# Kernel optimization log

Hardware: AMD Instinct MI355X
Metric: run time of the kernel (lower is better)

## Reference

```python
import jax, jax.numpy as jnp
import numpy as np

D, DK, DV, H, DFF = 1024, 64, 64, 16, 4096
B, LD, LE = 8, 1024, 1024
NEG = -1e9


def _ln(x, g, b, eps=1e-5):
    m = jnp.mean(x, axis=-1, keepdims=True)
    v = jnp.var(x, axis=-1, keepdims=True)
    return (x - m) / jnp.sqrt(v + eps) * g + b


def _mha(q_src, kv_src, wq, bq, wk, bk, wv, bv, mask):
    # wq/wk: [H, D, DK], wv: [H, D, DV]; per-head linear projections (with bias)
    Q = jnp.einsum('bld,hdk->bhlk', q_src, wq) + bq[:, None, :]
    K = jnp.einsum('bld,hdk->bhlk', kv_src, wk) + bk[:, None, :]
    V = jnp.einsum('bld,hdv->bhlv', kv_src, wv) + bv[:, None, :]
    s = jnp.einsum('bhqk,bhmk->bhqm', Q, K) / jnp.sqrt(jnp.asarray(DK, Q.dtype))
    if mask is not None:
        s = s + mask
    a = jax.nn.softmax(s, axis=-1)
    o = jnp.einsum('bhqm,bhmv->bhqv', a, V)  # [B,H,L,DV]
    b_, h_, l_, dv_ = o.shape
    return jnp.transpose(o, (0, 2, 1, 3)).reshape(b_, l_, h_ * dv_)


def setup_inputs() -> dict:
    key = jax.random.key(0)
    ks = jax.random.split(key, 24)
    sc = 0.02
    inp = {
        'decoder_embedding': jax.random.normal(ks[0], (B, LD, D), jnp.float32),
        'encoder_output': jax.random.normal(ks[1], (B, LE, D), jnp.float32),
        # masked (self) attention heads, stacked over H
        'm_wq': jax.random.normal(ks[2], (H, D, DK)) * sc,
        'm_bq': jnp.zeros((H, DK)),
        'm_wk': jax.random.normal(ks[3], (H, D, DK)) * sc,
        'm_bk': jnp.zeros((H, DK)),
        'm_wv': jax.random.normal(ks[4], (H, D, DV)) * sc,
        'm_bv': jnp.zeros((H, DV)),
        # cross attention heads
        'c_wq': jax.random.normal(ks[5], (H, D, DK)) * sc,
        'c_bq': jnp.zeros((H, DK)),
        'c_wk': jax.random.normal(ks[6], (H, D, DK)) * sc,
        'c_bk': jnp.zeros((H, DK)),
        'c_wv': jax.random.normal(ks[7], (H, D, DV)) * sc,
        'c_bv': jnp.zeros((H, DV)),
        # FFN
        'ff_w1': jax.random.normal(ks[8], (D, DFF)) * sc,
        'ff_b1': jnp.zeros((DFF,)),
        'ff_w2': jax.random.normal(ks[9], (DFF, D)) * sc,
        'ff_b2': jnp.zeros((D,)),
        # LayerNorms (ln2 reused for the third norm, as in the source)
        'ln1_g': jnp.ones((D,)), 'ln1_b': jnp.zeros((D,)),
        'ln2_g': jnp.ones((D,)), 'ln2_b': jnp.zeros((D,)),
    }
    return inp


def reference(decoder_embedding, encoder_output,
              m_wq, m_bq, m_wk, m_bk, m_wv, m_bv,
              c_wq, c_bq, c_wk, c_bk, c_wv, c_bv,
              ff_w1, ff_b1, ff_w2, ff_b2,
              ln1_g, ln1_b, ln2_g, ln2_b):
    Ld = decoder_embedding.shape[1]
    causal = jnp.where(jnp.tril(jnp.ones((Ld, Ld), bool)), 0.0, NEG)[None, None]
    # masked self-attention + residual + LN1
    sa = _mha(decoder_embedding, decoder_embedding, m_wq, m_bq, m_wk, m_bk, m_wv, m_bv, causal)
    x = _ln(decoder_embedding + sa, ln1_g, ln1_b)
    # cross-attention (Q from decoder, K/V from encoder) + residual + LN2
    ca = _mha(x, encoder_output, c_wq, c_bq, c_wk, c_bk, c_wv, c_bv, None)
    x = _ln(x + ca, ln2_g, ln2_b)
    # FFN + residual + LN2 again (source reuses layer_norm2)
    ff = jnp.maximum(x @ ff_w1 + ff_b1, 0.0) @ ff_w2 + ff_b2
    return _ln(x + ff, ln2_g, ln2_b)
```

## Files before the change

kernel.cpp:

```cpp
#include <hip/hip_runtime.h>
#include <hip/hip_bf16.h>
#include <cstdint>

typedef __bf16 bf16x8 __attribute__((ext_vector_type(8)));
typedef __bf16 bf16x4 __attribute__((ext_vector_type(4)));
typedef short  short4v __attribute__((ext_vector_type(4)));
typedef _Float16 f16x4 __attribute__((ext_vector_type(4)));
typedef float f32x4 __attribute__((ext_vector_type(4)));

union U128 { uint4 u; __bf16 h[8]; };
union U64  { uint2 u; __bf16 h[4]; };
union PV4  { uint2 u; bf16x4 b; short4v s; f16x4 f; };

#define DMODEL 1024
#define NHEAD  16
#define DHEAD  64

#if __has_builtin(__builtin_amdgcn_mfma_f32_16x16x16_bf16)
#define PV_F16 0
__device__ __forceinline__ f32x4 mfma16(PV4 a, PV4 b, f32x4 c) {
  return __builtin_amdgcn_mfma_f32_16x16x16_bf16(a.b, b.b, c, 0, 0, 0);
}
#elif __has_builtin(__builtin_amdgcn_mfma_f32_16x16x16bf16_1k)
#define PV_F16 0
__device__ __forceinline__ f32x4 mfma16(PV4 a, PV4 b, f32x4 c) {
  return __builtin_amdgcn_mfma_f32_16x16x16bf16_1k(a.s, b.s, c, 0, 0, 0);
}
#else
#define PV_F16 1
__device__ __forceinline__ f32x4 mfma16(PV4 a, PV4 b, f32x4 c) {
  return __builtin_amdgcn_mfma_f32_16x16x16f16(a.f, b.f, c, 0, 0, 0);
}
#endif

__device__ __forceinline__ uint16_t pv_bits(__bf16 v) {
#if PV_F16
  union { _Float16 f; uint16_t u; } x; x.f = (_Float16)(float)v; return x.u;
#else
  union { __bf16 b; uint16_t u; } x; x.b = v; return x.u;
#endif
}

__device__ __forceinline__ PV4 pack4(float a, float b, float c, float d) {
  PV4 r;
#if PV_F16
  r.f = (f16x4){(_Float16)a, (_Float16)b, (_Float16)c, (_Float16)d};
#else
  r.b = (bf16x4){(__bf16)a, (__bf16)b, (__bf16)c, (__bf16)d};
#endif
  return r;
}

__device__ __forceinline__ void async_copy16(const void* g, void* l) {
  __builtin_amdgcn_global_load_lds(
      (const __attribute__((address_space(1))) void*)g,
      (__attribute__((address_space(3))) void*)l, 16, 0, 0);
}

__global__ __launch_bounds__(256) void k_cast2(const float* __restrict__ a,
    const float* __restrict__ b, __bf16* __restrict__ da,
    __bf16* __restrict__ db, int n) {
  int i = (blockIdx.x * 256 + threadIdx.x) * 4;
  const float* s = a; __bf16* d = da;
  if (i >= n) { s = b; d = db; i -= n; }
  float4 v = *(const float4*)(s + i);
  U64 o;
  o.h[0] = (__bf16)v.x; o.h[1] = (__bf16)v.y;
  o.h[2] = (__bf16)v.z; o.h[3] = (__bf16)v.w;
  *(uint2*)(d + i) = o.u;
}

__global__ __launch_bounds__(256) void k_pack(float* __restrict__ dst,
    const float* __restrict__ s0, const float* __restrict__ s1,
    const float* __restrict__ s2, int n) {
  int i = blockIdx.x * 256 + threadIdx.x;
  if (i < n) dst[i] = s0[i];
  else if (i < 2 * n) dst[i] = s1[i - n];
  else if (i < 3 * n) dst[i] = s2[i - 2 * n];
}

__global__ __launch_bounds__(256) void k_transpose(const float* __restrict__ src,
    __bf16* __restrict__ dst, int R, int C) {
  __shared__ __bf16 tile[32][33];
  src += (size_t)blockIdx.z * R * C;
  dst += (size_t)blockIdx.z * R * C;
  int c0 = blockIdx.x * 32, r0 = blockIdx.y * 32;
  int tx = threadIdx.x & 31, ty = threadIdx.x >> 5;
  for (int i = ty; i < 32; i += 8)
    tile[i][tx] = (__bf16)src[(size_t)(r0 + i) * C + (c0 + tx)];
  __syncthreads();
  for (int i = ty; i < 32; i += 8)
    dst[(size_t)(c0 + i) * R + (r0 + tx)] = tile[tx][i];
}

__global__ __launch_bounds__(256) void k_transpose3(const float* __restrict__ s0,
    const float* __restrict__ s1, const float* __restrict__ s2,
    __bf16* __restrict__ dst, int R, int C) {
  __shared__ __bf16 tile[32][33];
  int z = blockIdx.z;
  const float* src = (z < 16) ? s0 : (z < 32) ? s1 : s2;
  src += (size_t)(z & 15) * R * C;
  dst += (size_t)z * R * C;
  int c0 = blockIdx.x * 32, r0 = blockIdx.y * 32;
  int tx = threadIdx.x & 31, ty = threadIdx.x >> 5;
  for (int i = ty; i < 32; i += 8)
    tile[i][tx] = (__bf16)src[(size_t)(r0 + i) * C + (c0 + tx)];
  __syncthreads();
  for (int i = ty; i < 32; i += 8)
    dst[(size_t)(c0 + i) * R + (r0 + tx)] = tile[tx][i];
}

template<bool RELU, typename OutT>
__global__ __launch_bounds__(256, 3) void k_gemm(const __bf16* __restrict__ A,
    const __bf16* __restrict__ Bt, const float* __restrict__ bias,
    OutT* __restrict__ C, int M, int N, int K) {
  __shared__ __bf16 As[128][64];
  __shared__ __bf16 Bs[128][64];
  const int m0 = blockIdx.y * 128, n0 = blockIdx.x * 128;
  const int t = threadIdx.x;
  const int wave = t >> 6, lane = t & 63;
  const int wm = (wave & 1) * 64, wn = (wave >> 1) * 64;
  const int lrow = lane & 15, quad = lane >> 4;
  const int r8 = lane >> 3;
  const int gG = (lane & 7) ^ (r8 & 7);
  const __bf16* Ap[4]; const __bf16* Bp[4];
  __bf16* lA[4]; __bf16* lB[4];
  for (int j = 0; j < 4; j++) {
    int rr = wave * 8 + j * 32 + r8;
    Ap[j] = A  + (size_t)(m0 + rr) * K + gG * 8;
    Bp[j] = Bt + (size_t)(n0 + rr) * K + gG * 8;
    lA[j] = &As[wave * 8 + j * 32][0];
    lB[j] = &Bs[wave * 8 + j * 32][0];
  }
  f32x4 acc[4][4] = {};
  for (int k0 = 0; k0 < K; k0 += 64) {
    __syncthreads();
    for (int j = 0; j < 4; j++) {
      async_copy16(Ap[j] + k0, lA[j]);
      async_copy16(Bp[j] + k0, lB[j]);
    }
    __syncthreads();
    for (int ks = 0; ks < 2; ks++) {
      bf16x8 af[4], bfv[4];
      for (int i = 0; i < 4; i++) {
        int ra = wm + i * 16 + lrow, rb = wn + i * 16 + lrow;
        af[i]  = *(const bf16x8*)&As[ra][(((ks * 4 + quad) ^ (ra & 7))) * 8];
        bfv[i] = *(const bf16x8*)&Bs[rb][(((ks * 4 + quad) ^ (rb & 7))) * 8];
      }
      for (int mi = 0; mi < 4; mi++)
        for (int ni = 0; ni < 4; ni++)
          acc[mi][ni] = __builtin_amdgcn_mfma_f32_16x16x32_bf16(af[mi], bfv[ni], acc[mi][ni], 0, 0, 0);
    }
  }
  for (int ni = 0; ni < 4; ni++) {
    int col = n0 + wn + ni * 16 + lrow;
    float bv = bias[col];
    for (int mi = 0; mi < 4; mi++) {
      int row = m0 + wm + mi * 16 + quad * 4;
      for (int r = 0; r < 4; r++) {
        float v = acc[mi][ni][r] + bv;
        if (RELU) v = fmaxf(v, 0.f);
        C[(size_t)(row + r) * N + col] = (OutT)v;
      }
    }
  }
}

template<bool CAUSAL>
__global__ __launch_bounds__(256, 4) void k_attn(const __bf16* __restrict__ Q,
    const __bf16* __restrict__ Kg, const __bf16* __restrict__ Vg,
    float* __restrict__ O, int Lq, int Lk, int qs, int kvs) {
  __shared__ alignas(16) __bf16   Ks[2][64][72];
  __shared__ alignas(16) uint16_t Vt[2][64][72];
  const int t = threadIdx.x;
  const int wave = t >> 6, lane = t & 63;
  const int lrow = lane & 15, quad = lane >> 4;
  const int wm16 = wave * 16;
  int qt[2];
  if (CAUSAL) { qt[0] = blockIdx.x; qt[1] = gridDim.x * 2 - 1 - blockIdx.x; }
  else        { qt[0] = blockIdx.x * 2; qt[1] = qt[0] + 1; }
  const int b = blockIdx.y >> 4, h = blockIdx.y & 15;
  const __bf16* Qb = Q  + (size_t)b * Lq * qs  + h * DHEAD;
  const __bf16* Kb = Kg + (size_t)b * Lk * kvs + h * DHEAD;
  const __bf16* Vb = Vg + (size_t)b * Lk * kvs + h * DHEAD;
  const float qsc = 0.125f * 1.44269504f;
  bf16x8 qf[2][2];
  for (int f = 0; f < 2; f++)
    for (int ks = 0; ks < 2; ks++) {
      U128 u;
      u.u = *(const uint4*)(Qb + (size_t)(qt[f] * 64 + wm16 + lrow) * qs + ks * 32 + quad * 8);
      for (int j = 0; j < 8; j++) u.h[j] = (__bf16)((float)u.h[j] * qsc);
      qf[f][ks] = *(const bf16x8*)u.h;
    }
  const int nkt = CAUSAL ? (qt[1] + 1) : (Lk / 64);
  const int krow = t >> 3, kcol = (t & 7) * 8;
  const int vkk = t & 63;
  f32x4 acc_o[2][4] = {};
  float m_r[2] = {-1e30f, -1e30f}, l_r[2] = {0.f, 0.f};
  uint4 ka, ka2, va, va2;
  ka  = *(const uint4*)(Kb + (size_t)krow * kvs + kcol);
  ka2 = *(const uint4*)(Kb + (size_t)(krow + 32) * kvs + kcol);
  va  = *(const uint4*)(Vb + (size_t)vkk * kvs + wave * 8);
  va2 = *(const uint4*)(Vb + (size_t)vkk * kvs + (wave + 4) * 8);
  int c = 0;
  for (int kt = 0; kt < nkt; kt++) {
    const int kn = (kt + 1 < nkt) ? (kt + 1) * 64 : kt * 64;
    uint4 na  = *(const uint4*)(Kb + (size_t)(kn + krow) * kvs + kcol);
    uint4 na2 = *(const uint4*)(Kb + (size_t)(kn + krow + 32) * kvs + kcol);
    uint4 nv  = *(const uint4*)(Vb + (size_t)(kn + vkk) * kvs + wave * 8);
    uint4 nv2 = *(const uint4*)(Vb + (size_t)(kn + vkk) * kvs + (wave + 4) * 8);
    *(uint4*)&Ks[c][krow][kcol]      = ka;
    *(uint4*)&Ks[c][krow + 32][kcol] = ka2;
    { U128 u; u.u = va;  for (int j = 0; j < 8; j++) Vt[c][wave * 8 + j][vkk] = pv_bits(u.h[j]); }
    { U128 u; u.u = va2; for (int j = 0; j < 8; j++) Vt[c][(wave + 4) * 8 + j][vkk] = pv_bits(u.h[j]); }
    __syncthreads();
    for (int f = 0; f < 2; f++) {
      if (CAUSAL && kt > qt[f]) continue;
      f32x4 st[4] = {};
      for (int ks = 0; ks < 2; ks++)
        for (int nb = 0; nb < 4; nb++) {
          bf16x8 kf = *(const bf16x8*)&Ks[c][nb * 16 + lrow][ks * 32 + quad * 8];
          st[nb] = __builtin_amdgcn_mfma_f32_16x16x32_bf16(kf, qf[f][ks], st[nb], 0, 0, 0);
        }
      float pm = -1e30f;
      for (int nb = 0; nb < 4; nb++)
        for (int r = 0; r < 4; r++) {
          float s = st[nb][r];
          if (CAUSAL && kt == qt[f])
            if (nb * 16 + quad * 4 + r > wm16 + lrow) s = -1e30f;
          st[nb][r] = s;
          pm = fmaxf(pm, s);
        }
      pm = fmaxf(pm, __shfl_xor(pm, 16));
      pm = fmaxf(pm, __shfl_xor(pm, 32));
      float mn = fmaxf(m_r[f], pm);
      float alpha = exp2f(m_r[f] - mn);
      m_r[f] = mn;
      float rs = 0.f;
      PV4 pf[4];
      for (int nb = 0; nb < 4; nb++) {
        float p0 = exp2f(st[nb][0] - mn), p1 = exp2f(st[nb][1] - mn);
        float p2 = exp2f(st[nb][2] - mn), p3 = exp2f(st[nb][3] - mn);
        rs += (p0 + p1) + (p2 + p3);
        pf[nb] = pack4(p0, p1, p2, p3);
      }
      rs += __shfl_xor(rs, 16);
      rs += __shfl_xor(rs, 32);
      l_r[f] = l_r[f] * alpha + rs;
      for (int ni = 0; ni < 4; ni++)
        for (int r = 0; r < 4; r++) acc_o[f][ni][r] *= alpha;
      for (int nb = 0; nb < 4; nb++)
        for (int ni = 0; ni < 4; ni++) {
          PV4 vf; vf.u = *(const uint2*)&Vt[c][ni * 16 + lrow][nb * 16 + quad * 4];
          acc_o[f][ni] = mfma16(vf, pf[nb], acc_o[f][ni]);
        }
    }
    ka = na; ka2 = na2; va = nv; va2 = nv2;
    c ^= 1;
  }
  for (int f = 0; f < 2; f++) {
    const float linv = 1.f / fmaxf(l_r[f], 1e-30f);
    float* orow = O + (size_t)b * Lq * DMODEL
                + (size_t)(qt[f] * 64 + wm16 + lrow) * DMODEL + h * DHEAD;
    for (int ni = 0; ni < 4; ni++) {
      float4 v = { acc_o[f][ni][0] * linv, acc_o[f][ni][1] * linv,
                   acc_o[f][ni][2] * linv, acc_o[f][ni][3] * linv };
      *(float4*)(orow + ni * 16 + quad * 4) = v;
    }
  }
}

template<typename ResT, typename OutT>
__global__ __launch_bounds__(256) void k_ln_add(const ResT* __restrict__ a,
    const float* __restrict__ bres, const float* __restrict__ g,
    const float* __restrict__ be, OutT* __restrict__ out) {
  __shared__ float red[2][4];
  const int r = blockIdx.x, t = threadIdx.x;
  const size_t base = (size_t)r * DMODEL + t * 4;
  float x[4];
  for (int i = 0; i < 4; i++) x[i] = (float)a[base + i] + bres[base + i];
  float s  = x[0] + x[1] + x[2] + x[3];
  float s2 = x[0]*x[0] + x[1]*x[1] + x[2]*x[2] + x[3]*x[3];
  for (int off = 32; off > 0; off >>= 1) {
    s  += __shfl_down(s, off);
    s2 += __shfl_down(s2, off);
  }
  if ((t & 63) == 0) { red[0][t >> 6] = s; red[1][t >> 6] = s2; }
  __syncthreads();
  s  = red[0][0] + red[0][1] + red[0][2] + red[0][3];
  s2 = red[1][0] + red[1][1] + red[1][2] + red[1][3];
  const float mean = s * (1.f / DMODEL);
  const float var  = s2 * (1.f / DMODEL) - mean * mean;
  const float rstd = rsqrtf(var + 1e-5f);
  for (int i = 0; i < 4; i++)
    out[base + i] = (OutT)((x[i] - mean) * rstd * g[t * 4 + i] + be[t * 4 + i]);
}

extern "C" void kernel_launch(void* const* d_in, const int* in_sizes, int n_in,
                              void* d_out, int out_size, void* d_ws, size_t ws_size,
                              hipStream_t stream) {
  (void)in_sizes; (void)n_in; (void)out_size; (void)ws_size;
  const float* dec   = (const float*)d_in[0];
  const float* enc   = (const float*)d_in[1];
  const float* m_wq  = (const float*)d_in[2];
  const float* m_bq  = (const float*)d_in[3];
  const float* m_wk  = (const float*)d_in[4];
  const float* m_bk  = (const float*)d_in[5];
  const float* m_wv  = (const float*)d_in[6];
  const float* m_bv  = (const float*)d_in[7];
  const float* c_wq  = (const float*)d_in[8];
  const float* c_bq  = (const float*)d_in[9];
  const float* c_wk  = (const float*)d_in[10];
  const float* c_bk  = (const float*)d_in[11];
  const float* c_wv  = (const float*)d_in[12];
  const float* c_bv  = (const float*)d_in[13];
  const float* ff_w1 = (const float*)d_in[14];
  const float* ff_b1 = (const float*)d_in[15];
  const float* ff_w2 = (const float*)d_in[16];
  const float* ff_b2 = (const float*)d_in[17];
  const float* ln1_g = (const float*)d_in[18];
  const float* ln1_b = (const float*)d_in[19];
  const float* ln2_g = (const float*)d_in[20];
  const float* ln2_b = (const float*)d_in[21];

  char* w = (char*)d_ws;
  __bf16* decB = (__bf16*)(w);
  __bf16* encB = (__bf16*)(w + (16ull << 20));
  __bf16* X1b  = decB;
  __bf16* X2b  = encB;
  __bf16* WB   = (__bf16*)(w + (32ull << 20));
  float*  BP   = (float*) (w + (38ull << 20));
  __bf16* QKV  = (__bf16*)(w + (40ull << 20));
  __bf16* KV   = (__bf16*)(w + (40ull << 20));
  __bf16* Qc   = (__bf16*)(w + (72ull << 20));
  __bf16* FF   = (__bf16*)(w + (40ull << 20));
  float*  AO   = (float*) (w + (104ull << 20));
  float* out = (float*)d_out;

  const int M = 8192, NTOK = M * DMODEL;
  dim3 blk(256);
  dim3 gT3(2, 32, 48);
  dim3 gA(8, 128);
  dim3 gL(M);

  k_cast2<<<dim3(2 * NTOK / 1024), blk, 0, stream>>>(dec, enc, decB, encB, NTOK);

  k_transpose3<<<gT3, blk, 0, stream>>>(m_wq, m_wk, m_wv, WB, 1024, 64);
  k_pack<<<dim3(12), blk, 0, stream>>>(BP, m_bq, m_bk, m_bv, 1024);
  k_gemm<false, __bf16><<<dim3(24, 64), blk, 0, stream>>>(decB, WB, BP, QKV, M, 3072, 1024);
  k_attn<true><<<gA, blk, 0, stream>>>(QKV, QKV + 1024, QKV + 2048, AO, 1024, 1024, 3072, 3072);
  k_ln_add<float, __bf16><<<gL, blk, 0, stream>>>(dec, AO, ln1_g, ln1_b, X1b);

  k_transpose3<<<gT3, blk, 0, stream>>>(c_wk, c_wv, c_wq, WB, 1024, 64);
  k_pack<<<dim3(8), blk, 0, stream>>>(BP, c_bk, c_bv, c_bv, 1024);
  k_gemm<false, __bf16><<<dim3(16, 64), blk, 0, stream>>>(encB, WB, BP, KV, M, 2048, 1024);
  k_gemm<false, __bf16><<<dim3(8, 64), blk, 0, stream>>>(X1b, WB + (2 << 20), c_bq, Qc, M, 1024, 1024);
  k_attn<false><<<gA, blk, 0, stream>>>(Qc, KV, KV + 1024, AO, 1024, 1024, 1024, 2048);
  k_ln_add<__bf16, __bf16><<<gL, blk, 0, stream>>>(X1b, AO, ln2_g, ln2_b, X2b);

  k_transpose<<<dim3(128, 32, 1), blk, 0, stream>>>(ff_w1, WB, 1024, 4096);
  k_gemm<true, __bf16><<<dim3(32, 64), blk, 0, stream>>>(X2b, WB, ff_b1, FF, M, 4096, 1024);
  k_transpose<<<dim3(32, 128, 1), blk, 0, stream>>>(ff_w2, WB, 4096, 1024);
  k_gemm<false, float><<<dim3(8, 64), blk, 0, stream>>>(FF, WB, ff_b2, AO, M, 1024, 4096);
  k_ln_add<__bf16, float><<<gL, blk, 0, stream>>>(X2b, AO, ln2_g, ln2_b, out);
}
```

Measured before the change: 653.9 us.

## Pre-transpose V in a separate kernel and read it directly from global in attention

Adds a k_vt kernel that writes V per (batch, head) in a transposed [DHEAD][L] layout into a new workspace region. The attention kernel drops its shared-memory V tile, along with the per-element LDS transpose and V prefetch, and loads PV MFMA operands straight from global memory. This removes LDS scatter stores and halves shared-memory use, which may raise occupancy. The cost is two extra transpose launches and uncoalesced 8-byte global loads in the inner loop, which rely on L2/L1 hits and are no longer prefetched. The VT buffer at offset 88MB must not overlap Qc (72MB + 16MB), and it ends exactly at 88MB.

```diff
diff --git a/kernel.cpp b/kernel.cpp
--- a/kernel.cpp
+++ b/kernel.cpp
@@ -108,6 +108,21 @@
   __syncthreads();
   for (int i = ty; i < 32; i += 8)
     dst[(size_t)(c0 + i) * R + (r0 + tx)] = tile[tx][i];
+}
+
+__global__ __launch_bounds__(256) void k_vt(const __bf16* __restrict__ V,
+    uint16_t* __restrict__ VT, int L, int kvs) {
+  __shared__ uint16_t tile[32][33];
+  const int z = blockIdx.z, b = z >> 4, h = z & 15;
+  const __bf16* src = V + (size_t)b * L * kvs + h * DHEAD;
+  uint16_t* dst = VT + (size_t)z * DHEAD * L;
+  const int l0 = blockIdx.x * 32, d0 = blockIdx.y * 32;
+  const int tx = threadIdx.x & 31, ty = threadIdx.x >> 5;
+  for (int i = ty; i < 32; i += 8)
+    tile[i][tx] = pv_bits(src[(size_t)(l0 + i) * kvs + d0 + tx]);
+  __syncthreads();
+  for (int i = ty; i < 32; i += 8)
+    dst[(size_t)(d0 + i) * L + l0 + tx] = tile[tx][i];
 }
 
 template<bool RELU, typename OutT>
@@ -168,10 +183,9 @@
 
 template<bool CAUSAL>
 __global__ __launch_bounds__(256, 4) void k_attn(const __bf16* __restrict__ Q,
-    const __bf16* __restrict__ Kg, const __bf16* __restrict__ Vg,
+    const __bf16* __restrict__ Kg, const uint16_t* __restrict__ VT,
     float* __restrict__ O, int Lq, int Lk, int qs, int kvs) {
-  __shared__ alignas(16) __bf16   Ks[2][64][72];
-  __shared__ alignas(16) uint16_t Vt[2][64][72];
+  __shared__ alignas(16) __bf16 Ks[2][64][72];
   const int t = threadIdx.x;
   const int wave = t >> 6, lane = t & 63;
   const int lrow = lane & 15, quad = lane >> 4;
@@ -182,7 +196,7 @@
   const int b = blockIdx.y >> 4, h = blockIdx.y & 15;
   const __bf16* Qb = Q  + (size_t)b * Lq * qs  + h * DHEAD;
   const __bf16* Kb = Kg + (size_t)b * Lk * kvs + h * DHEAD;
-  const __bf16* Vb = Vg + (size_t)b * Lk * kvs + h * DHEAD;
+  const uint16_t* VTb = VT + (size_t)blockIdx.y * DHEAD * Lk;
   const float qsc = 0.125f * 1.44269504f;
   bf16x8 qf[2][2];
   for (int f = 0; f < 2; f++)
@@ -194,25 +208,18 @@
     }
   const int nkt = CAUSAL ? (qt[1] + 1) : (Lk / 64);
   const int krow = t >> 3, kcol = (t & 7) * 8;
-  const int vkk = t & 63;
   f32x4 acc_o[2][4] = {};
   float m_r[2] = {-1e30f, -1e30f}, l_r[2] = {0.f, 0.f};
-  uint4 ka, ka2, va, va2;
+  uint4 ka, ka2;
   ka  = *(const uint4*)(Kb + (size_t)krow * kvs + kcol);
   ka2 = *(const uint4*)(Kb + (size_t)(krow + 32) * kvs + kcol);
-  va  = *(const uint4*)(Vb + (size_t)vkk * kvs + wave * 8);
-  va2 = *(const uint4*)(Vb + (size_t)vkk * kvs + (wave + 4) * 8);
   int c = 0;
   for (int kt = 0; kt < nkt; kt++) {
     const int kn = (kt + 1 < nkt) ? (kt + 1) * 64 : kt * 64;
     uint4 na  = *(const uint4*)(Kb + (size_t)(kn + krow) * kvs + kcol);
     uint4 na2 = *(const uint4*)(Kb + (size_t)(kn + krow + 32) * kvs + kcol);
-    uint4 nv  = *(const uint4*)(Vb + (size_t)(kn + vkk) * kvs + wave * 8);
-    uint4 nv2 = *(const uint4*)(Vb + (size_t)(kn + vkk) * kvs + (wave + 4) * 8);
     *(uint4*)&Ks[c][krow][kcol]      = ka;
     *(uint4*)&Ks[c][krow + 32][kcol] = ka2;
-    { U128 u; u.u = va;  for (int j = 0; j < 8; j++) Vt[c][wave * 8 + j][vkk] = pv_bits(u.h[j]); }
-    { U128 u; u.u = va2; for (int j = 0; j < 8; j++) Vt[c][(wave + 4) * 8 + j][vkk] = pv_bits(u.h[j]); }
     __syncthreads();
     for (int f = 0; f < 2; f++) {
       if (CAUSAL && kt > qt[f]) continue;
@@ -251,11 +258,13 @@
         for (int r = 0; r < 4; r++) acc_o[f][ni][r] *= alpha;
       for (int nb = 0; nb < 4; nb++)
         for (int ni = 0; ni < 4; ni++) {
-          PV4 vf; vf.u = *(const uint2*)&Vt[c][ni * 16 + lrow][nb * 16 + quad * 4];
+          PV4 vf;
+          vf.u = *(const uint2*)(VTb + (size_t)(ni * 16 + lrow) * Lk
+                                 + kt * 64 + nb * 16 + quad * 4);
           acc_o[f][ni] = mfma16(vf, pf[nb], acc_o[f][ni]);
         }
     }
-    ka = na; ka2 = na2; va = nv; va2 = nv2;
+    ka = na; ka2 = na2;
     c ^= 1;
   }
   for (int f = 0; f < 2; f++) {
@@ -334,6 +343,7 @@
   __bf16* KV   = (__bf16*)(w + (40ull << 20));
   __bf16* Qc   = (__bf16*)(w + (72ull << 20));
   __bf16* FF   = (__bf16*)(w + (40ull << 20));
+  uint16_t* VTw = (uint16_t*)(w + (88ull << 20));
   float*  AO   = (float*) (w + (104ull << 20));
   float* out = (float*)d_out;
 
@@ -341,6 +351,7 @@
   dim3 blk(256);
   dim3 gT3(2, 32, 48);
   dim3 gA(8, 128);
+  dim3 gV(32, 2, 128);
   dim3 gL(M);
 
   k_cast2<<<dim3(2 * NTOK / 1024), blk, 0, stream>>>(dec, enc, decB, encB, NTOK);
@@ -348,14 +359,16 @@
   k_transpose3<<<gT3, blk, 0, stream>>>(m_wq, m_wk, m_wv, WB, 1024, 64);
   k_pack<<<dim3(12), blk, 0, stream>>>(BP, m_bq, m_bk, m_bv, 1024);
   k_gemm<false, __bf16><<<dim3(24, 64), blk, 0, stream>>>(decB, WB, BP, QKV, M, 3072, 1024);
-  k_attn<true><<<gA, blk, 0, stream>>>(QKV, QKV + 1024, QKV + 2048, AO, 1024, 1024, 3072, 3072);
+  k_vt<<<gV, blk, 0, stream>>>(QKV + 2048, VTw, 1024, 3072);
+  k_attn<true><<<gA, blk, 0, stream>>>(QKV, QKV + 1024, VTw, AO, 1024, 1024, 3072, 3072);
   k_ln_add<float, __bf16><<<gL, blk, 0, stream>>>(dec, AO, ln1_g, ln1_b, X1b);
 
   k_transpose3<<<gT3, blk, 0, stream>>>(c_wk, c_wv, c_wq, WB, 1024, 64);
   k_pack<<<dim3(8), blk, 0, stream>>>(BP, c_bk, c_bv, c_bv, 1024);
   k_gemm<false, __bf16><<<dim3(16, 64), blk, 0, stream>>>(encB, WB, BP, KV, M, 2048, 1024);
+  k_vt<<<gV, blk, 0, stream>>>(KV + 1024, VTw, 1024, 2048);
   k_gemm<false, __bf16><<<dim3(8, 64), blk, 0, stream>>>(X1b, WB + (2 << 20), c_bq, Qc, M, 1024, 1024);
-  k_attn<false><<<gA, blk, 0, stream>>>(Qc, KV, KV + 1024, AO, 1024, 1024, 1024, 2048);
+  k_attn<false><<<gA, blk, 0, stream>>>(Qc, KV, VTw, AO, 1024, 1024, 1024, 2048);
   k_ln_add<__bf16, __bf16><<<gL, blk, 0, stream>>>(X1b, AO, ln2_g, ln2_b, X2b);
 
   k_transpose<<<dim3(128, 32, 1), blk, 0, stream>>>(ff_w1, WB, 1024, 4096);
```

Measured after the change: 811.6 us. 24.1% more time.

## Add 256x256-tile 8-wave GEMM with staged async prefetch for wide projections

Applied to the files above, without the earlier changes.

Introduces a new GEMM kernel that uses 256x256 output tiles with 512 threads (8 waves, each computing 128x64). It double-buffers LDS with XOR-swizzled layout and interleaves async global-to-LDS copies between MFMA phases, raising wave priority around the MFMA bursts. It is used for the self-attention QKV, cross K/V and FFN1 GEMMs, which raises data reuse per block and reduces global traffic. The cost is large LDS and register use per block, fewer blocks in the grid, and tail-wave imbalance on the smaller grids.

```diff
diff --git a/kernel.cpp b/kernel.cpp
--- a/kernel.cpp
+++ b/kernel.cpp
@@ -164,6 +164,123 @@
       }
     }
   }
+}
+
+template<bool RELU, typename OutT>
+__global__ __launch_bounds__(512, 2) void k_gemm2(const __bf16* __restrict__ A,
+    const __bf16* __restrict__ Bt, const float* __restrict__ bias,
+    OutT* __restrict__ C, int M, int N, int K) {
+  __shared__ __bf16 As[2][256][64];
+  __shared__ __bf16 Bs[2][256][64];
+  const int m0 = blockIdx.y * 256, n0 = blockIdx.x * 256;
+  const int t = threadIdx.x;
+  const int wid = t >> 6, lane = t & 63;
+  const int wr = wid >> 2, wc = wid & 3;
+  const int lrow = lane & 15, quad = lane >> 4;
+  const int r8 = lane >> 3;
+  const int gG = (lane & 7) ^ (r8 & 7);
+  const __bf16* aS[4]; const __bf16* bS[4];
+  #pragma unroll
+  for (int s = 0; s < 4; s++) {
+    const int row = s * 64 + wid * 8 + r8;
+    aS[s] = A  + (size_t)(m0 + row) * K + gG * 8;
+    bS[s] = Bt + (size_t)(n0 + row) * K + gG * 8;
+  }
+#define STG_A(c_, s_, kt_) async_copy16(aS[s_] + (size_t)(kt_) * 64, &As[c_][(s_) * 64 + wid * 8][0])
+#define STG_B(c_, s_, kt_) async_copy16(bS[s_] + (size_t)(kt_) * 64, &Bs[c_][(s_) * 64 + wid * 8][0])
+#define LDA2(c_, mi_, ks_) ({ const int ra_ = wr * 128 + (mi_) * 16 + lrow; \
+    *(const bf16x8*)&As[c_][ra_][(((ks_) * 4 + quad) ^ (ra_ & 7)) * 8]; })
+#define LDB2(c_, ni_, ks_) ({ const int rb_ = wc * 64 + (ni_) * 16 + lrow; \
+    *(const bf16x8*)&Bs[c_][rb_][(((ks_) * 4 + quad) ^ (rb_ & 7)) * 8]; })
+#define GBAR __builtin_amdgcn_s_barrier()
+#define LGKM0 { asm volatile("s_waitcnt lgkmcnt(0)" ::: "memory"); __builtin_amdgcn_sched_barrier(0); }
+  f32x4 acc[8][4] = {};
+  const int nt = K >> 6;
+  STG_A(0, 0, 0); STG_A(0, 1, 0); STG_A(0, 2, 0); STG_A(0, 3, 0);
+  STG_B(0, 0, 0); STG_B(0, 1, 0); STG_B(0, 2, 0); STG_B(0, 3, 0);
+  STG_B(1, 0, 1); STG_B(1, 1, 1);
+  asm volatile("s_waitcnt vmcnt(2)" ::: "memory");
+  GBAR;
+  for (int kt = 0; kt < nt; kt++) {
+    const int c = kt & 1, d = c ^ 1;
+    const bool st1 = (kt + 1 < nt), st2 = (kt + 2 < nt);
+    bf16x8 a[4], b[4];
+    #pragma unroll
+    for (int ni = 0; ni < 4; ni++) b[ni] = LDB2(c, ni, 0);
+    #pragma unroll
+    for (int mi = 0; mi < 4; mi++) a[mi] = LDA2(c, mi, 0);
+    if (st1) { STG_A(d, 0, kt + 1); STG_A(d, 1, kt + 1); }
+    GBAR; LGKM0;
+    __builtin_amdgcn_s_setprio(1);
+    #pragma unroll
+    for (int mi = 0; mi < 4; mi++)
+      #pragma unroll
+      for (int ni = 0; ni < 4; ni++)
+        acc[mi][ni] = __builtin_amdgcn_mfma_f32_16x16x32_bf16(a[mi], b[ni], acc[mi][ni], 0, 0, 0);
+    __builtin_amdgcn_s_setprio(0);
+    GBAR;
+    #pragma unroll
+    for (int mi = 0; mi < 4; mi++) a[mi] = LDA2(c, mi + 4, 0);
+    if (st1) { STG_A(d, 2, kt + 1); STG_A(d, 3, kt + 1); }
+    GBAR; LGKM0;
+    __builtin_amdgcn_s_setprio(1);
+    #pragma unroll
+    for (int mi = 0; mi < 4; mi++)
+      #pragma unroll
+      for (int ni = 0; ni < 4; ni++)
+        acc[mi + 4][ni] = __builtin_amdgcn_mfma_f32_16x16x32_bf16(a[mi], b[ni], acc[mi + 4][ni], 0, 0, 0);
+    __builtin_amdgcn_s_setprio(0);
+    GBAR;
+    #pragma unroll
+    for (int ni = 0; ni < 4; ni++) b[ni] = LDB2(c, ni, 1);
+    #pragma unroll
+    for (int mi = 0; mi < 4; mi++) a[mi] = LDA2(c, mi, 1);
+    if (st1) { STG_B(d, 2, kt + 1); STG_B(d, 3, kt + 1); }
+    GBAR; LGKM0;
+    __builtin_amdgcn_s_setprio(1);
+    #pragma unroll
+    for (int mi = 0; mi < 4; mi++)
+      #pragma unroll
+      for (int ni = 0; ni < 4; ni++)
+        acc[mi][ni] = __builtin_amdgcn_mfma_f32_16x16x32_bf16(a[mi], b[ni], acc[mi][ni], 0, 0, 0);
+    __builtin_amdgcn_s_setprio(0);
+    GBAR;
+    #pragma unroll
+    for (int mi = 0; mi < 4; mi++) a[mi] = LDA2(c, mi + 4, 1);
+    if (st2) { STG_B(c, 0, kt + 2); STG_B(c, 1, kt + 2); }
+    GBAR; LGKM0;
+    __builtin_amdgcn_s_setprio(1);
+    #pragma unroll
+    for (int mi = 0; mi < 4; mi++)
+      #pragma unroll
+      for (int ni = 0; ni < 4; ni++)
+        acc[mi + 4][ni] = __builtin_amdgcn_mfma_f32_16x16x32_bf16(a[mi], b[ni], acc[mi + 4][ni], 0, 0, 0);
+    __builtin_amdgcn_s_setprio(0);
+    if (st2) { asm volatile("s_waitcnt vmcnt(2)" ::: "memory"); }
+    else     { asm volatile("s_waitcnt vmcnt(0)" ::: "memory"); }
+    GBAR;
+  }
+  #pragma unroll
+  for (int ni = 0; ni < 4; ni++) {
+    const int col = n0 + wc * 64 + ni * 16 + lrow;
+    const float bv = bias[col];
+    #pragma unroll
+    for (int mi = 0; mi < 8; mi++) {
+      const int row = m0 + wr * 128 + mi * 16 + quad * 4;
+      #pragma unroll
+      for (int r = 0; r < 4; r++) {
+        float v = acc[mi][ni][r] + bv;
+        if (RELU) v = fmaxf(v, 0.f);
+        C[(size_t)(row + r) * N + col] = (OutT)v;
+      }
+    }
+  }
+#undef STG_A
+#undef STG_B
+#undef LDA2
+#undef LDB2
+#undef GBAR
+#undef LGKM0
 }
 
 template<bool CAUSAL>
@@ -339,6 +456,7 @@
 
   const int M = 8192, NTOK = M * DMODEL;
   dim3 blk(256);
+  dim3 blk2(512);
   dim3 gT3(2, 32, 48);
   dim3 gA(8, 128);
   dim3 gL(M);
@@ -347,19 +465,19 @@
 
   k_transpose3<<<gT3, blk, 0, stream>>>(m_wq, m_wk, m_wv, WB, 1024, 64);
   k_pack<<<dim3(12), blk, 0, stream>>>(BP, m_bq, m_bk, m_bv, 1024);
-  k_gemm<false, __bf16><<<dim3(24, 64), blk, 0, stream>>>(decB, WB, BP, QKV, M, 3072, 1024);
+  k_gemm2<false, __bf16><<<dim3(12, 32), blk2, 0, stream>>>(decB, WB, BP, QKV, M, 3072, 1024);
   k_attn<true><<<gA, blk, 0, stream>>>(QKV, QKV + 1024, QKV + 2048, AO, 1024, 1024, 3072, 3072);
   k_ln_add<float, __bf16><<<gL, blk, 0, stream>>>(dec, AO, ln1_g, ln1_b, X1b);
 
   k_transpose3<<<gT3, blk, 0, stream>>>(c_wk, c_wv, c_wq, WB, 1024, 64);
   k_pack<<<dim3(8), blk, 0, stream>>>(BP, c_bk, c_bv, c_bv, 1024);
-  k_gemm<false, __bf16><<<dim3(16, 64), blk, 0, stream>>>(encB, WB, BP, KV, M, 2048, 1024);
+  k_gemm2<false, __bf16><<<dim3(8, 32), blk2, 0, stream>>>(encB, WB, BP, KV, M, 2048, 1024);
   k_gemm<false, __bf16><<<dim3(8, 64), blk, 0, stream>>>(X1b, WB + (2 << 20), c_bq, Qc, M, 1024, 1024);
   k_attn<false><<<gA, blk, 0, stream>>>(Qc, KV, KV + 1024, AO, 1024, 1024, 1024, 2048);
   k_ln_add<__bf16, __bf16><<<gL, blk, 0, stream>>>(X1b, AO, ln2_g, ln2_b, X2b);
 
   k_transpose<<<dim3(128, 32, 1), blk, 0, stream>>>(ff_w1, WB, 1024, 4096);
-  k_gemm<true, __bf16><<<dim3(32, 64), blk, 0, stream>>>(X2b, WB, ff_b1, FF, M, 4096, 1024);
+  k_gemm2<true, __bf16><<<dim3(16, 32), blk2, 0, stream>>>(X2b, WB, ff_b1, FF, M, 4096, 1024);
   k_transpose<<<dim3(32, 128, 1), blk, 0, stream>>>(ff_w2, WB, 4096, 1024);
   k_gemm<false, float><<<dim3(8, 64), blk, 0, stream>>>(FF, WB, ff_b2, AO, M, 1024, 4096);
   k_ln_add<__bf16, float><<<gL, blk, 0, stream>>>(X2b, AO, ln2_g, ln2_b, out);
```

Result: slower. 691.7 us (+5.8%).
